# Kernel tuning notes

Hardware: AMD Instinct MI355X
Metric: run time of the kernel (lower is better)

Reference implementation:

```python
import jax, jax.numpy as jnp
import numpy as np

HID = 128  # hidden_channel
C = 256    # feat_channel

def conv1x1(x, w, b):
    # x: [N, Cin, H, W], w: [Cout, Cin], b: [Cout]
    return jnp.einsum('nchw,oc->nohw', x, w) + b[None, :, None, None]

def maxpool2(x):
    N, Ch, H, W = x.shape
    return x.reshape(N, Ch, H // 2, 2, W // 2, 2).max(axis=(3, 5))

def setup_inputs() -> dict:
    key = jax.random.key(0)
    ks = jax.random.split(key, 6)
    rois = jax.random.normal(ks[0], (128, C, 14, 14), dtype=jnp.float32)
    feature = jax.random.normal(ks[1], (2, C, 64, 64), dtype=jnp.float32)
    s_in = 1.0 / np.sqrt(C)
    s_hid = 1.0 / np.sqrt(HID)
    wq = jax.random.uniform(ks[2], (HID, C), minval=-s_in, maxval=s_in, dtype=jnp.float32)
    wk = jax.random.uniform(ks[3], (HID, C), minval=-s_in, maxval=s_in, dtype=jnp.float32)
    wv = jax.random.uniform(ks[4], (HID, C), minval=-s_in, maxval=s_in, dtype=jnp.float32)
    wre = jax.random.uniform(ks[5], (C, HID), minval=-s_hid, maxval=s_hid, dtype=jnp.float32)
    return {
        'rois': rois, 'feature': feature,
        'wq': wq, 'bq': jnp.zeros((HID,), jnp.float32),
        'wk': wk, 'bk': jnp.zeros((HID,), jnp.float32),
        'wv': wv, 'bv': jnp.zeros((HID,), jnp.float32),
        'wre': wre, 'bre': jnp.zeros((C,), jnp.float32),
    }

def reference(rois, feature, wq, bq, wk, bk, wv, bv, wre, bre):
    BS_roinum, Cf, h, w = rois.shape
    BS = feature.shape[0]
    roinum = BS_roinum // BS
    _h, _w = h // 2, w // 2

    # Q at full resolution
    q = conv1x1(rois, wq, bq)                              # [BS*R, HID, h, w]
    q = q.transpose(0, 2, 3, 1).reshape(BS, roinum * h * w, HID)

    ds = maxpool2(rois)                                    # [BS*R, C, _h, _w]
    k = conv1x1(ds, wk, bk).transpose(0, 2, 3, 1).reshape(BS, roinum * _h * _w, HID)
    v = conv1x1(ds, wv, bv).transpose(0, 2, 3, 1).reshape(BS, roinum * _h * _w, HID)

    score = jnp.einsum('bqc,bkc->bqk', q, k)               # [BS, R*h*w, R*_h*_w]
    score = jax.nn.softmax(score, axis=-1)
    y = jnp.einsum('bqk,bkc->bqc', score, v)               # [BS, R*h*w, HID]

    y = y.reshape(BS * roinum, h, w, HID).transpose(0, 3, 1, 2)
    y = conv1x1(y, wre, bre)                               # [BS*R, C, h, w]
    return rois + y
```

## Files before the change

### kernel.cpp

```cpp
#include <hip/hip_runtime.h>
#include <math.h>

constexpr int CIN  = 256;
constexpr int HID  = 128;
constexpr int P    = 196;
constexpr int PP   = 49;
constexpr int NQ   = 12544;
constexpr int NKEY = 3136;
constexpr int NS   = 5;

using f32x4 = __attribute__((ext_vector_type(4))) float;
using s16x8 = __attribute__((ext_vector_type(8))) short;
using s16x4 = __attribute__((ext_vector_type(4))) short;
using u32x2 = __attribute__((ext_vector_type(2))) unsigned int;

#define GLOBAL_AS(p) ((const void __attribute__((address_space(1)))*)(p))
#define LDS_AS(p)    ((void __attribute__((address_space(3)))*)(p))

__device__ __forceinline__ unsigned short f2bf(float x) {
    unsigned int u = __float_as_uint(x);
    u += 0x7FFFu + ((u >> 16) & 1u);
    return (unsigned short)(u >> 16);
}
__device__ __forceinline__ float bf2f(unsigned short s) {
    return __uint_as_float(((unsigned int)s) << 16);
}

__global__ __launch_bounds__(256) void prep_kernel(
    const float* __restrict__ rois,
    const float* __restrict__ wq, const float* __restrict__ wk,
    const float* __restrict__ wv, const float* __restrict__ wre,
    unsigned short* __restrict__ xkv,
    unsigned short* __restrict__ wqb, unsigned short* __restrict__ wkb,
    unsigned short* __restrict__ wvb, unsigned short* __restrict__ wreb)
{
    const int bx = blockIdx.x;
    const int t  = threadIdx.x;

    if (bx >= 512) {
        const int which = bx - 512;
        const float* src = (which == 0) ? wq : (which == 1) ? wk : (which == 2) ? wv : wre;
        unsigned short* dst = (which == 0) ? wqb : (which == 1) ? wkb
                             : (which == 2) ? wvb : wreb;
        #pragma unroll 4
        for (int i = 0; i < 32; ++i) {
            const int idx = i * 256 + t;
            const float4 v = ((const float4*)src)[idx];
            s16x4 o;
            o[0] = (short)f2bf(v.x); o[1] = (short)f2bf(v.y);
            o[2] = (short)f2bf(v.z); o[3] = (short)f2bf(v.w);
            *(s16x4*)(dst + idx * 4) = o;
        }
        return;
    }

    const int n = bx >> 2;
    const int g = bx & 3;
    const int b = n >> 6, r = n & 63;
    __shared__ float xT[196 * 68];

    const int c_loc = t >> 2;
    const int pq    = t & 3;

    const float4* row4 = (const float4*)(rois + ((size_t)n * CIN + g * 64 + c_loc) * P);
    #pragma unroll
    for (int j = 0; j < 13; ++j) {
        const int idx4 = pq + 4 * j;
        if (idx4 < 49) {
            const float4 v = row4[idx4];
            xT[(idx4 * 4 + 0) * 68 + c_loc] = v.x;
            xT[(idx4 * 4 + 1) * 68 + c_loc] = v.y;
            xT[(idx4 * 4 + 2) * 68 + c_loc] = v.z;
            xT[(idx4 * 4 + 3) * 68 + c_loc] = v.w;
        }
    }
    __syncthreads();

    #pragma unroll
    for (int i = 0; i < 2; ++i) {
        const int u = i * 256 + t;
        if (u < 392) {
            const int pp = u >> 3, ch8 = (u & 7) * 8;
            const int py = pp / 7, px_ = pp - py * 7;
            const int base00 = (py * 2) * 14 + px_ * 2;
            s16x8 o;
            #pragma unroll
            for (int e = 0; e < 8; ++e) {
                const int c = ch8 + e;
                const float m0 = fmaxf(xT[(base00)      * 68 + c], xT[(base00 + 1)  * 68 + c]);
                const float m1 = fmaxf(xT[(base00 + 14) * 68 + c], xT[(base00 + 15) * 68 + c]);
                o[e] = (short)f2bf(fmaxf(m0, m1));
            }
            *(s16x8*)(xkv + ((size_t)b * NKEY + r * PP + pp) * CIN + g * 64 + ch8) = o;
        }
    }
}

__global__ __launch_bounds__(128) void gemm_fused_kernel(
    const float* __restrict__ rois, const unsigned short* __restrict__ xkv,
    const unsigned short* __restrict__ wqb, const unsigned short* __restrict__ wkb,
    const unsigned short* __restrict__ wvb,
    const float* __restrict__ bq, const float* __restrict__ bk, const float* __restrict__ bv,
    unsigned short* __restrict__ q, unsigned short* __restrict__ kmat,
    unsigned short* __restrict__ vt_g)
{
    const int bx = blockIdx.x;
    const int t = threadIdx.x;
    const int wid = t >> 6, lane = t & 63;
    const int quad = lane >> 4, c = lane & 15;

    __shared__ unsigned short xT[64 * 264];

    f32x4 acc[4][4];
    #pragma unroll
    for (int i = 0; i < 4; ++i)
        #pragma unroll
        for (int j = 0; j < 4; ++j) acc[i][j] = (f32x4)(0.f);

    if (bx < 392) {
        const int m0 = bx * 64;
        {
            const int c_loc = t >> 2;
            const int pq4   = t & 3;
            const int sw    = pq4 << 3;
            #pragma unroll
            for (int ci = 0; ci < 8; ++ci) {
                const int ch = ci * 32 + c_loc;
                #pragma unroll
                for (int j = 0; j < 4; ++j) {
                    const int idx4 = (m0 >> 2) + pq4 + 4 * j;
                    const int n_img = idx4 / 49;
                    const int p4 = idx4 - n_img * 49;
                    const float4 v = ((const float4*)(rois + ((size_t)(n_img * CIN + ch)) * P))[p4];
                    const int r0 = (pq4 + 4 * j) * 4;
                    const int cs = ch ^ sw;
                    xT[(r0 + 0) * 264 + cs] = f2bf(v.x);
                    xT[(r0 + 1) * 264 + cs] = f2bf(v.y);
                    xT[(r0 + 2) * 264 + cs] = f2bf(v.z);
                    xT[(r0 + 3) * 264 + cs] = f2bf(v.w);
                }
            }
        }
        __syncthreads();

        const int m_base = m0;
        const int n_base = wid * 64;
        const int swr = ((c >> 2) & 3) << 3;
        #pragma unroll
        for (int ks = 0; ks < 8; ++ks) {
            s16x8 af[4], bf[4];
            #pragma unroll
            for (int mt = 0; mt < 4; ++mt)
                af[mt] = *(const s16x8*)&xT[(mt * 16 + c) * 264 + ((ks * 32 + quad * 8) ^ swr)];
            #pragma unroll
            for (int nt = 0; nt < 4; ++nt)
                bf[nt] = *(const s16x8*)(wqb + (size_t)(n_base + nt * 16 + c) * CIN + ks * 32 + quad * 8);
            #pragma unroll
            for (int mt = 0; mt < 4; ++mt)
                #pragma unroll
                for (int nt = 0; nt < 4; ++nt)
                    acc[mt][nt] = __builtin_amdgcn_mfma_f32_16x16x32_bf16(bf[nt], af[mt], acc[mt][nt], 0, 0, 0);
        }
        #pragma unroll
        for (int mt = 0; mt < 4; ++mt) {
            const int m = m_base + mt * 16 + c;
            #pragma unroll
            for (int nt = 0; nt < 4; ++nt) {
                const int n0 = n_base + nt * 16 + quad * 4;
                const float4 b4 = *(const float4*)&bq[n0];
                s16x4 o4;
                o4[0] = (short)f2bf(acc[mt][nt][0] + b4.x);
                o4[1] = (short)f2bf(acc[mt][nt][1] + b4.y);
                o4[2] = (short)f2bf(acc[mt][nt][2] + b4.z);
                o4[3] = (short)f2bf(acc[mt][nt][3] + b4.w);
                *(s16x4*)(q + (size_t)m * HID + n0) = o4;
            }
        }
        return;
    }

    const unsigned short* w; const float* bias;
    int m_blk, mode;
    if (bx < 490) { mode = 1; w = wkb; bias = bk; m_blk = bx - 392; }
    else          { mode = 2; w = wvb; bias = bv; m_blk = bx - 490; }
    const int m_base = m_blk * 64;
    const int n_base = wid * 64;

    if (mode == 1) {
        #pragma unroll
        for (int ks = 0; ks < 8; ++ks) {
            s16x8 af[4], bf[4];
            #pragma unroll
            for (int mt = 0; mt < 4; ++mt)
                af[mt] = *(const s16x8*)(xkv + (size_t)(m_base + mt * 16 + c) * CIN + ks * 32 + quad * 8);
            #pragma unroll
            for (int nt = 0; nt < 4; ++nt)
                bf[nt] = *(const s16x8*)(w + (size_t)(n_base + nt * 16 + c) * CIN + ks * 32 + quad * 8);
            #pragma unroll
            for (int mt = 0; mt < 4; ++mt)
                #pragma unroll
                for (int nt = 0; nt < 4; ++nt)
                    acc[mt][nt] = __builtin_amdgcn_mfma_f32_16x16x32_bf16(bf[nt], af[mt], acc[mt][nt], 0, 0, 0);
        }
        #pragma unroll
        for (int mt = 0; mt < 4; ++mt) {
            const int m = m_base + mt * 16 + c;
            #pragma unroll
            for (int nt = 0; nt < 4; ++nt) {
                const int n0 = n_base + nt * 16 + quad * 4;
                const float4 b4 = *(const float4*)&bias[n0];
                s16x4 o4;
                o4[0] = (short)f2bf(acc[mt][nt][0] + b4.x);
                o4[1] = (short)f2bf(acc[mt][nt][1] + b4.y);
                o4[2] = (short)f2bf(acc[mt][nt][2] + b4.z);
                o4[3] = (short)f2bf(acc[mt][nt][3] + b4.w);
                *(s16x4*)(kmat + (size_t)m * HID + n0) = o4;
            }
        }
    } else {
        #pragma unroll
        for (int ks = 0; ks < 8; ++ks) {
            s16x8 af[4], bf[4];
            #pragma unroll
            for (int mt = 0; mt < 4; ++mt)
                af[mt] = *(const s16x8*)(xkv + (size_t)(m_base + mt * 16 + c) * CIN + ks * 32 + quad * 8);
            #pragma unroll
            for (int nt = 0; nt < 4; ++nt)
                bf[nt] = *(const s16x8*)(w + (size_t)(n_base + nt * 16 + c) * CIN + ks * 32 + quad * 8);
            #pragma unroll
            for (int mt = 0; mt < 4; ++mt)
                #pragma unroll
                for (int nt = 0; nt < 4; ++nt)
                    acc[mt][nt] = __builtin_amdgcn_mfma_f32_16x16x32_bf16(af[mt], bf[nt], acc[mt][nt], 0, 0, 0);
        }
        #pragma unroll
        for (int nt = 0; nt < 4; ++nt) {
            const int d = n_base + nt * 16 + c;
            const float bv_ = bias[d];
            #pragma unroll
            for (int mt = 0; mt < 4; ++mt) {
                const int key0 = m_base + mt * 16 + quad * 4;
                const int bb = (key0 >= NKEY) ? 1 : 0;
                const int kl = key0 - bb * NKEY;
                s16x4 o4;
                #pragma unroll
                for (int rr = 0; rr < 4; ++rr)
                    o4[rr] = (short)f2bf(acc[mt][nt][rr] + bv_);
                *(s16x4*)(vt_g + ((size_t)bb * HID + d) * NKEY + kl) = o4;
            }
        }
    }
}

__global__ __launch_bounds__(256, 2) void attn_kernel(
    const unsigned short* __restrict__ q, const unsigned short* __restrict__ kmat,
    const unsigned short* __restrict__ vt_g,
    unsigned short* __restrict__ opart, float* __restrict__ lpart)
{
    const int fid  = blockIdx.x;
    const int xcd  = fid & 7, slot = fid >> 3;
    const int wg   = (xcd < 2 ? xcd * 62 : 124 + (xcd - 2) * 61) + slot;
    const int g    = wg / NS;
    const int s    = wg - g * NS;
    const int qblk = g % 49;
    const int b    = g / 49;

    const int tid  = threadIdx.x;
    const int w    = tid >> 6;
    const int lane = tid & 63;
    const int quad = lane >> 4;
    const int c    = lane & 15;
    const int qb   = qblk * 256 + w * 64;

    __shared__ unsigned short Kst[2][32 * 128];
    __shared__ unsigned short Vst[2][128 * 32];
    __shared__ unsigned short Ps[4][64 * 72];

    const unsigned short* qg = q    + (size_t)b * NQ   * HID;
    const unsigned short* kg = kmat + (size_t)b * NKEY * HID;
    const unsigned short* vt = vt_g + (size_t)b * HID  * NKEY;

    int koff[2], voff[2];
    #pragma unroll
    for (int i = 0; i < 2; ++i) {
        const int dstk = w * 2048 + (i * 64 + lane) * 16;
        koff[i] = dstk ^ (((dstk >> 8) & 7) << 4);
        const int chunk = i * 64 + lane;
        const int d = w * 32 + (chunk >> 2), sl = chunk & 3;
        voff[i] = d * (NKEY * 2) + ((sl ^ (d & 3)) * 16);
    }
    const char* kc = (const char*)kg;
    const char* vc = (const char*)vt;

    const int B6[6] = {0, 20, 40, 60, 79, 98};
    const int kt0 = B6[s], kt1 = B6[s + 1];

    {
        const char* ks_ = kc + (size_t)kt0 * 8192;
        const char* vs_ = vc + (size_t)kt0 * 64;
        #pragma unroll
        for (int i = 0; i < 2; ++i) {
            __builtin_amdgcn_global_load_lds(GLOBAL_AS(ks_ + koff[i]),
                LDS_AS((char*)&Kst[0][0] + w * 2048 + i * 1024), 16, 0, 0);
            __builtin_amdgcn_global_load_lds(GLOBAL_AS(vs_ + voff[i]),
                LDS_AS((char*)&Vst[0][0] + w * 2048 + i * 1024), 16, 0, 0);
        }
    }

    s16x8 qf[4][4];
    #pragma unroll
    for (int nt = 0; nt < 4; ++nt)
        #pragma unroll
        for (int ks = 0; ks < 4; ++ks)
            qf[nt][ks] = *(const s16x8*)(qg + (size_t)(qb + nt * 16 + c) * HID + ks * 32 + quad * 8);

    f32x4 Ob[4][8];
    #pragma unroll
    for (int nt = 0; nt < 4; ++nt)
        #pragma unroll
        for (int nd = 0; nd < 8; ++nd) Ob[nt][nd] = (f32x4)(0.f);
    float l[4] = {0.f, 0.f, 0.f, 0.f};

    __syncthreads();

    int buf = 0;
    for (int kt = kt0; kt < kt1; ++kt) {
        if (kt + 1 < kt1) {
            const char* ks_ = kc + (size_t)(kt + 1) * 8192;
            const char* vs_ = vc + (size_t)(kt + 1) * 64;
            #pragma unroll
            for (int i = 0; i < 2; ++i) {
                __builtin_amdgcn_global_load_lds(GLOBAL_AS(ks_ + koff[i]),
                    LDS_AS((char*)&Kst[buf ^ 1][0] + w * 2048 + i * 1024), 16, 0, 0);
                __builtin_amdgcn_global_load_lds(GLOBAL_AS(vs_ + voff[i]),
                    LDS_AS((char*)&Vst[buf ^ 1][0] + w * 2048 + i * 1024), 16, 0, 0);
            }
        }

        const char* Kb = (const char*)&Kst[buf][0];
        const char* Vb = (const char*)&Vst[buf][0];

        f32x4 st[2][4];
        #pragma unroll
        for (int mt = 0; mt < 2; ++mt)
            #pragma unroll
            for (int nt = 0; nt < 4; ++nt) st[mt][nt] = (f32x4)(0.f);
        #pragma unroll
        for (int mt = 0; mt < 2; ++mt) {
            const int row = mt * 16 + c;
            s16x8 kf[4];
            #pragma unroll
            for (int ks = 0; ks < 4; ++ks)
                kf[ks] = *(const s16x8*)(Kb + ((row * 256 + ks * 64 + quad * 16) ^ ((c & 7) << 4)));
            #pragma unroll
            for (int ks = 0; ks < 4; ++ks)
                #pragma unroll
                for (int nt = 0; nt < 4; ++nt)
                    st[mt][nt] = __builtin_amdgcn_mfma_f32_16x16x32_bf16(kf[ks], qf[nt][ks], st[mt][nt], 0, 0, 0);
        }

        #pragma unroll
        for (int mt = 0; mt < 2; ++mt) {
            #pragma unroll
            for (int nt = 0; nt < 4; ++nt) {
                const float e0 = __expf(st[mt][nt][0]);
                const float e1 = __expf(st[mt][nt][1]);
                const float e2 = __expf(st[mt][nt][2]);
                const float e3 = __expf(st[mt][nt][3]);
                l[nt] += (e0 + e1) + (e2 + e3);
                u32x2 pk;
                pk[0] = (unsigned int)f2bf(e0) | ((unsigned int)f2bf(e1) << 16);
                pk[1] = (unsigned int)f2bf(e2) | ((unsigned int)f2bf(e3) << 16);
                *(u32x2*)&Ps[w][(nt * 16 + c) * 72 + mt * 16 + quad * 4] = pk;
            }
        }

        s16x8 pf[4];
        #pragma unroll
        for (int nt = 0; nt < 4; ++nt)
            pf[nt] = *(const s16x8*)&Ps[w][(nt * 16 + c) * 72 + quad * 8];
        #pragma unroll
        for (int g2 = 0; g2 < 2; ++g2) {
            s16x8 vf[4];
            #pragma unroll
            for (int dd = 0; dd < 4; ++dd) {
                const int d = (g2 * 4 + dd) * 16 + c;
                vf[dd] = *(const s16x8*)(Vb + (d * 64 + ((quad ^ (d & 3)) * 16)));
            }
            #pragma unroll
            for (int dd = 0; dd < 4; ++dd)
                #pragma unroll
                for (int nt = 0; nt < 4; ++nt)
                    Ob[nt][g2 * 4 + dd] = __builtin_amdgcn_mfma_f32_16x16x32_bf16(pf[nt], vf[dd], Ob[nt][g2 * 4 + dd], 0, 0, 0);
        }

        if (kt + 1 < kt1) __syncthreads();
        buf ^= 1;
    }

    unsigned short* Op = opart + (size_t)(s * 2 + b) * NQ * HID;
    #pragma unroll
    for (int nt = 0; nt < 4; ++nt) {
        #pragma unroll
        for (int nd = 0; nd < 8; ++nd) {
            #pragma unroll
            for (int rr = 0; rr < 4; ++rr) {
                const int qrow = qb + nt * 16 + quad * 4 + rr;
                Op[(size_t)qrow * HID + nd * 16 + c] = f2bf(Ob[nt][nd][rr]);
            }
        }
    }
    #pragma unroll
    for (int nt = 0; nt < 4; ++nt) {
        l[nt] += __shfl_xor(l[nt], 16, 64);
        l[nt] += __shfl_xor(l[nt], 32, 64);
    }
    if (quad == 0) {
        float* lp = lpart + (size_t)(s * 2 + b) * NQ;
        #pragma unroll
        for (int nt = 0; nt < 4; ++nt) lp[qb + nt * 16 + c] = l[nt];
    }
}

__global__ __launch_bounds__(256) void outproj_kernel(
    const float* __restrict__ rois,
    const unsigned short* __restrict__ opart, const float* __restrict__ lpart,
    const unsigned short* __restrict__ wreb, const float* __restrict__ bre,
    float* __restrict__ out)
{
    const int t = threadIdx.x;
    const int wid = t >> 6, lane = t & 63;
    const int quad = lane >> 4, c = lane & 15;
    const int m0 = blockIdx.x * 64;
    const int b  = (m0 >= NQ) ? 1 : 0;

    __shared__ unsigned short ys[64 * 136];

    {
        const int m_loc = t >> 2, kq = t & 3;
        const int q_local = (m0 + m_loc) - b * NQ;
        float lsum = 0.f;
        #pragma unroll
        for (int sl = 0; sl < NS; ++sl)
            lsum += lpart[(size_t)(sl * 2 + b) * NQ + q_local];
        const float invl = 1.0f / lsum;
        #pragma unroll
        for (int ch = 0; ch < 4; ++ch) {
            float a8[8] = {0, 0, 0, 0, 0, 0, 0, 0};
            #pragma unroll
            for (int sl = 0; sl < NS; ++sl) {
                const s16x8 v = *(const s16x8*)&opart[
                    ((size_t)(sl * 2 + b) * NQ + q_local) * HID + kq * 32 + ch * 8];
                #pragma unroll
                for (int e = 0; e < 8; ++e) a8[e] += bf2f((unsigned short)v[e]);
            }
            s16x8 o;
            #pragma unroll
            for (int e = 0; e < 8; ++e) o[e] = (short)f2bf(a8[e] * invl);
            *(s16x8*)&ys[m_loc * 136 + kq * 32 + ch * 8] = o;
        }
    }
    __syncthreads();

    const int o_base = wid * 64;
    s16x8 wf[4][4];
    #pragma unroll
    for (int ot = 0; ot < 4; ++ot)
        #pragma unroll
        for (int ks = 0; ks < 4; ++ks)
            wf[ot][ks] = *(const s16x8*)(wreb + (size_t)(o_base + ot * 16 + c) * HID + ks * 32 + quad * 8);

    f32x4 acc[4][4];
    #pragma unroll
    for (int i = 0; i < 4; ++i)
        #pragma unroll
        for (int j = 0; j < 4; ++j) acc[i][j] = (f32x4)(0.f);

    #pragma unroll
    for (int ks = 0; ks < 4; ++ks) {
        s16x8 yf[4];
        #pragma unroll
        for (int mt = 0; mt < 4; ++mt)
            yf[mt] = *(const s16x8*)&ys[(mt * 16 + c) * 136 + ks * 32 + quad * 8];
        #pragma unroll
        for (int mt = 0; mt < 4; ++mt)
            #pragma unroll
            for (int ot = 0; ot < 4; ++ot)
                acc[mt][ot] = __builtin_amdgcn_mfma_f32_16x16x32_bf16(yf[mt], wf[ot][ks], acc[mt][ot], 0, 0, 0);
    }

    #pragma unroll
    for (int ot = 0; ot < 4; ++ot) {
        const int o = o_base + ot * 16 + c;
        const float br = bre[o];
        #pragma unroll
        for (int mt = 0; mt < 4; ++mt) {
            const int m_g = m0 + mt * 16 + quad * 4;
            const int mm  = m_g - b * NQ;
            const int r_roi = mm / 196;
            const int p     = mm - r_roi * 196;
            const int n_img = b * 64 + r_roi;
            const size_t base = ((size_t)n_img * CIN + o) * P + p;
            const float4 rv = *(const float4*)&rois[base];
            float4 ov;
            ov.x = rv.x + br + acc[mt][ot][0];
            ov.y = rv.y + br + acc[mt][ot][1];
            ov.z = rv.z + br + acc[mt][ot][2];
            ov.w = rv.w + br + acc[mt][ot][3];
            *(float4*)&out[base] = ov;
        }
    }
}

extern "C" void kernel_launch(void* const* d_in, const int* in_sizes, int n_in,
                              void* d_out, int out_size, void* d_ws, size_t ws_size,
                              hipStream_t stream)
{
    (void)in_sizes; (void)n_in; (void)out_size; (void)ws_size;
    const float* rois = (const float*)d_in[0];
    const float* wq  = (const float*)d_in[2];
    const float* bq  = (const float*)d_in[3];
    const float* wk  = (const float*)d_in[4];
    const float* bk  = (const float*)d_in[5];
    const float* wv  = (const float*)d_in[6];
    const float* bv  = (const float*)d_in[7];
    const float* wre = (const float*)d_in[8];
    const float* bre = (const float*)d_in[9];
    float* out = (float*)d_out;

    char* ws = (char*)d_ws;
    unsigned short* opart = (unsigned short*)(ws);
    unsigned short* xkv   = (unsigned short*)(ws + 12845056);
    unsigned short* wqb   = (unsigned short*)(ws + 16056320);
    unsigned short* wkb   = (unsigned short*)(ws + 16121856);
    unsigned short* wvb   = (unsigned short*)(ws + 16187392);
    unsigned short* q     = (unsigned short*)(ws + 32112640);
    unsigned short* kmat  = (unsigned short*)(ws + 38535168);
    unsigned short* vt_g  = (unsigned short*)(ws + 40140800);
    float*          lpart = (float*)         (ws + 41746432);
    unsigned short* wreb  = (unsigned short*)(ws + 42248192);

    prep_kernel<<<dim3(516), 256, 0, stream>>>(rois, wq, wk, wv, wre,
                                               xkv, wqb, wkb, wvb, wreb);
    gemm_fused_kernel<<<dim3(588), 128, 0, stream>>>(rois, xkv, wqb, wkb, wvb,
                                                     bq, bk, bv, q, kmat, vt_g);
    attn_kernel<<<dim3(490), 256, 0, stream>>>(q, kmat, vt_g, opart, lpart);
    outproj_kernel<<<dim3(392), 256, 0, stream>>>(rois, opart, lpart, wreb, bre, out);
}
```

Baseline: 191.2 us.

## Fuse maxpool and weight conversion into projection GEMM kernel, drop prep launch

Removes the separate prep kernel. The K/V projection blocks now max-pool one ROI directly from fp32 rois into swizzled LDS, and every GEMM converts fp32 weights to bf16 on the fly, while one extra block converts wre. This saves a kernel launch and the global round trip through the pooled xkv buffer. In exchange, weight bf16 conversion is repeated in every block, K/V tiles of 49 rows waste part of the 64-row MFMA tile, and the V-transpose stores become scalar.

```diff
diff --git a/kernel.cpp b/kernel.cpp
--- a/kernel.cpp
+++ b/kernel.cpp
@@ -26,86 +26,30 @@
     return __uint_as_float(((unsigned int)s) << 16);
 }
 
-__global__ __launch_bounds__(256) void prep_kernel(
+__global__ __launch_bounds__(128) void gemm_fused_kernel(
     const float* __restrict__ rois,
     const float* __restrict__ wq, const float* __restrict__ wk,
     const float* __restrict__ wv, const float* __restrict__ wre,
-    unsigned short* __restrict__ xkv,
-    unsigned short* __restrict__ wqb, unsigned short* __restrict__ wkb,
-    unsigned short* __restrict__ wvb, unsigned short* __restrict__ wreb)
+    const float* __restrict__ bq, const float* __restrict__ bk, const float* __restrict__ bv,
+    unsigned short* __restrict__ q, unsigned short* __restrict__ kmat,
+    unsigned short* __restrict__ vt_g, unsigned short* __restrict__ wreb)
 {
     const int bx = blockIdx.x;
-    const int t  = threadIdx.x;
-
-    if (bx >= 512) {
-        const int which = bx - 512;
-        const float* src = (which == 0) ? wq : (which == 1) ? wk : (which == 2) ? wv : wre;
-        unsigned short* dst = (which == 0) ? wqb : (which == 1) ? wkb
-                             : (which == 2) ? wvb : wreb;
+    const int t = threadIdx.x;
+
+    if (bx == 648) {
         #pragma unroll 4
-        for (int i = 0; i < 32; ++i) {
-            const int idx = i * 256 + t;
-            const float4 v = ((const float4*)src)[idx];
+        for (int i = 0; i < 64; ++i) {
+            const int idx = i * 128 + t;
+            const float4 v = ((const float4*)wre)[idx];
             s16x4 o;
             o[0] = (short)f2bf(v.x); o[1] = (short)f2bf(v.y);
             o[2] = (short)f2bf(v.z); o[3] = (short)f2bf(v.w);
-            *(s16x4*)(dst + idx * 4) = o;
+            *(s16x4*)(wreb + idx * 4) = o;
         }
         return;
     }
 
-    const int n = bx >> 2;
-    const int g = bx & 3;
-    const int b = n >> 6, r = n & 63;
-    __shared__ float xT[196 * 68];
-
-    const int c_loc = t >> 2;
-    const int pq    = t & 3;
-
-    const float4* row4 = (const float4*)(rois + ((size_t)n * CIN + g * 64 + c_loc) * P);
-    #pragma unroll
-    for (int j = 0; j < 13; ++j) {
-        const int idx4 = pq + 4 * j;
-        if (idx4 < 49) {
-            const float4 v = row4[idx4];
-            xT[(idx4 * 4 + 0) * 68 + c_loc] = v.x;
-            xT[(idx4 * 4 + 1) * 68 + c_loc] = v.y;
-            xT[(idx4 * 4 + 2) * 68 + c_loc] = v.z;
-            xT[(idx4 * 4 + 3) * 68 + c_loc] = v.w;
-        }
-    }
-    __syncthreads();
-
-    #pragma unroll
-    for (int i = 0; i < 2; ++i) {
-        const int u = i * 256 + t;
-        if (u < 392) {
-            const int pp = u >> 3, ch8 = (u & 7) * 8;
-            const int py = pp / 7, px_ = pp - py * 7;
-            const int base00 = (py * 2) * 14 + px_ * 2;
-            s16x8 o;
-            #pragma unroll
-            for (int e = 0; e < 8; ++e) {
-                const int c = ch8 + e;
-                const float m0 = fmaxf(xT[(base00)      * 68 + c], xT[(base00 + 1)  * 68 + c]);
-                const float m1 = fmaxf(xT[(base00 + 14) * 68 + c], xT[(base00 + 15) * 68 + c]);
-                o[e] = (short)f2bf(fmaxf(m0, m1));
-            }
-            *(s16x8*)(xkv + ((size_t)b * NKEY + r * PP + pp) * CIN + g * 64 + ch8) = o;
-        }
-    }
-}
-
-__global__ __launch_bounds__(128) void gemm_fused_kernel(
-    const float* __restrict__ rois, const unsigned short* __restrict__ xkv,
-    const unsigned short* __restrict__ wqb, const unsigned short* __restrict__ wkb,
-    const unsigned short* __restrict__ wvb,
-    const float* __restrict__ bq, const float* __restrict__ bk, const float* __restrict__ bv,
-    unsigned short* __restrict__ q, unsigned short* __restrict__ kmat,
-    unsigned short* __restrict__ vt_g)
-{
-    const int bx = blockIdx.x;
-    const int t = threadIdx.x;
     const int wid = t >> 6, lane = t & 63;
     const int quad = lane >> 4, c = lane & 15;
 
@@ -116,6 +60,9 @@
     for (int i = 0; i < 4; ++i)
         #pragma unroll
         for (int j = 0; j < 4; ++j) acc[i][j] = (f32x4)(0.f);
+
+    const int n_base = wid * 64;
+    const int swr = ((c >> 2) & 3) << 3;
 
     if (bx < 392) {
         const int m0 = bx * 64;
@@ -143,9 +90,6 @@
         }
         __syncthreads();
 
-        const int m_base = m0;
-        const int n_base = wid * 64;
-        const int swr = ((c >> 2) & 3) << 3;
         #pragma unroll
         for (int ks = 0; ks < 8; ++ks) {
             s16x8 af[4], bf[4];
@@ -153,8 +97,17 @@
             for (int mt = 0; mt < 4; ++mt)
                 af[mt] = *(const s16x8*)&xT[(mt * 16 + c) * 264 + ((ks * 32 + quad * 8) ^ swr)];
             #pragma unroll
-            for (int nt = 0; nt < 4; ++nt)
-                bf[nt] = *(const s16x8*)(wqb + (size_t)(n_base + nt * 16 + c) * CIN + ks * 32 + quad * 8);
+            for (int nt = 0; nt < 4; ++nt) {
+                const float* wp = wq + (size_t)(n_base + nt * 16 + c) * CIN + ks * 32 + quad * 8;
+                const float4 w0 = *(const float4*)wp;
+                const float4 w1 = *(const float4*)(wp + 4);
+                s16x8 bv8;
+                bv8[0] = (short)f2bf(w0.x); bv8[1] = (short)f2bf(w0.y);
+                bv8[2] = (short)f2bf(w0.z); bv8[3] = (short)f2bf(w0.w);
+                bv8[4] = (short)f2bf(w1.x); bv8[5] = (short)f2bf(w1.y);
+                bv8[6] = (short)f2bf(w1.z); bv8[7] = (short)f2bf(w1.w);
+                bf[nt] = bv8;
+            }
             #pragma unroll
             for (int mt = 0; mt < 4; ++mt)
                 #pragma unroll
@@ -163,7 +116,7 @@
         }
         #pragma unroll
         for (int mt = 0; mt < 4; ++mt) {
-            const int m = m_base + mt * 16 + c;
+            const int m = m0 + mt * 16 + c;
             #pragma unroll
             for (int nt = 0; nt < 4; ++nt) {
                 const int n0 = n_base + nt * 16 + quad * 4;
@@ -179,12 +132,28 @@
         return;
     }
 
-    const unsigned short* w; const float* bias;
-    int m_blk, mode;
-    if (bx < 490) { mode = 1; w = wkb; bias = bk; m_blk = bx - 392; }
-    else          { mode = 2; w = wvb; bias = bv; m_blk = bx - 490; }
-    const int m_base = m_blk * 64;
-    const int n_base = wid * 64;
+    const int mode = (bx < 520) ? 1 : 2;
+    const int n_roi = bx - ((mode == 1) ? 392 : 520);
+    const int b = n_roi >> 6, r = n_roi & 63;
+    {
+        #pragma unroll
+        for (int i = 0; i < 16; ++i) {
+            const int unit = i * 128 + t;
+            const int ch = unit >> 3, py = unit & 7;
+            if (py < 7) {
+                const float* ra = rois + ((size_t)n_roi * CIN + ch) * P + py * 28;
+                #pragma unroll
+                for (int px = 0; px < 7; ++px) {
+                    const float2 a = *(const float2*)(ra + px * 2);
+                    const float2 bb = *(const float2*)(ra + 14 + px * 2);
+                    const float m = fmaxf(fmaxf(a.x, a.y), fmaxf(bb.x, bb.y));
+                    const int pp = py * 7 + px;
+                    xT[pp * 264 + (ch ^ (((pp >> 2) & 3) << 3))] = f2bf(m);
+                }
+            }
+        }
+    }
+    __syncthreads();
 
     if (mode == 1) {
         #pragma unroll
@@ -192,10 +161,19 @@
             s16x8 af[4], bf[4];
             #pragma unroll
             for (int mt = 0; mt < 4; ++mt)
-                af[mt] = *(const s16x8*)(xkv + (size_t)(m_base + mt * 16 + c) * CIN + ks * 32 + quad * 8);
-            #pragma unroll
-            for (int nt = 0; nt < 4; ++nt)
-                bf[nt] = *(const s16x8*)(w + (size_t)(n_base + nt * 16 + c) * CIN + ks * 32 + quad * 8);
+                af[mt] = *(const s16x8*)&xT[(mt * 16 + c) * 264 + ((ks * 32 + quad * 8) ^ swr)];
+            #pragma unroll
+            for (int nt = 0; nt < 4; ++nt) {
+                const float* wp = wk + (size_t)(n_base + nt * 16 + c) * CIN + ks * 32 + quad * 8;
+                const float4 w0 = *(const float4*)wp;
+                const float4 w1 = *(const float4*)(wp + 4);
+                s16x8 bv8;
+                bv8[0] = (short)f2bf(w0.x); bv8[1] = (short)f2bf(w0.y);
+                bv8[2] = (short)f2bf(w0.z); bv8[3] = (short)f2bf(w0.w);
+                bv8[4] = (short)f2bf(w1.x); bv8[5] = (short)f2bf(w1.y);
+                bv8[6] = (short)f2bf(w1.z); bv8[7] = (short)f2bf(w1.w);
+                bf[nt] = bv8;
+            }
             #pragma unroll
             for (int mt = 0; mt < 4; ++mt)
                 #pragma unroll
@@ -204,17 +182,20 @@
         }
         #pragma unroll
         for (int mt = 0; mt < 4; ++mt) {
-            const int m = m_base + mt * 16 + c;
-            #pragma unroll
-            for (int nt = 0; nt < 4; ++nt) {
-                const int n0 = n_base + nt * 16 + quad * 4;
-                const float4 b4 = *(const float4*)&bias[n0];
-                s16x4 o4;
-                o4[0] = (short)f2bf(acc[mt][nt][0] + b4.x);
-                o4[1] = (short)f2bf(acc[mt][nt][1] + b4.y);
-                o4[2] = (short)f2bf(acc[mt][nt][2] + b4.z);
-                o4[3] = (short)f2bf(acc[mt][nt][3] + b4.w);
-                *(s16x4*)(kmat + (size_t)m * HID + n0) = o4;
+            const int m = mt * 16 + c;
+            if (mt < 3 || c == 0) {
+                const size_t krow = (size_t)(b * NKEY + r * 49 + m) * HID;
+                #pragma unroll
+                for (int nt = 0; nt < 4; ++nt) {
+                    const int n0 = n_base + nt * 16 + quad * 4;
+                    const float4 b4 = *(const float4*)&bk[n0];
+                    s16x4 o4;
+                    o4[0] = (short)f2bf(acc[mt][nt][0] + b4.x);
+                    o4[1] = (short)f2bf(acc[mt][nt][1] + b4.y);
+                    o4[2] = (short)f2bf(acc[mt][nt][2] + b4.z);
+                    o4[3] = (short)f2bf(acc[mt][nt][3] + b4.w);
+                    *(s16x4*)(kmat + krow + n0) = o4;
+                }
             }
         }
     } else {
@@ -223,10 +204,19 @@
             s16x8 af[4], bf[4];
             #pragma unroll
             for (int mt = 0; mt < 4; ++mt)
-                af[mt] = *(const s16x8*)(xkv + (size_t)(m_base + mt * 16 + c) * CIN + ks * 32 + quad * 8);
-            #pragma unroll
-            for (int nt = 0; nt < 4; ++nt)
-                bf[nt] = *(const s16x8*)(w + (size_t)(n_base + nt * 16 + c) * CIN + ks * 32 + quad * 8);
+                af[mt] = *(const s16x8*)&xT[(mt * 16 + c) * 264 + ((ks * 32 + quad * 8) ^ swr)];
+            #pragma unroll
+            for (int nt = 0; nt < 4; ++nt) {
+                const float* wp = wv + (size_t)(n_base + nt * 16 + c) * CIN + ks * 32 + quad * 8;
+                const float4 w0 = *(const float4*)wp;
+                const float4 w1 = *(const float4*)(wp + 4);
+                s16x8 bv8;
+                bv8[0] = (short)f2bf(w0.x); bv8[1] = (short)f2bf(w0.y);
+                bv8[2] = (short)f2bf(w0.z); bv8[3] = (short)f2bf(w0.w);
+                bv8[4] = (short)f2bf(w1.x); bv8[5] = (short)f2bf(w1.y);
+                bv8[6] = (short)f2bf(w1.z); bv8[7] = (short)f2bf(w1.w);
+                bf[nt] = bv8;
+            }
             #pragma unroll
             for (int mt = 0; mt < 4; ++mt)
                 #pragma unroll
@@ -236,17 +226,18 @@
         #pragma unroll
         for (int nt = 0; nt < 4; ++nt) {
             const int d = n_base + nt * 16 + c;
-            const float bv_ = bias[d];
+            const float bv_ = bv[d];
+            const size_t vrow = ((size_t)b * HID + d) * NKEY + r * 49;
             #pragma unroll
             for (int mt = 0; mt < 4; ++mt) {
-                const int key0 = m_base + mt * 16 + quad * 4;
-                const int bb = (key0 >= NKEY) ? 1 : 0;
-                const int kl = key0 - bb * NKEY;
-                s16x4 o4;
-                #pragma unroll
-                for (int rr = 0; rr < 4; ++rr)
-                    o4[rr] = (short)f2bf(acc[mt][nt][rr] + bv_);
-                *(s16x4*)(vt_g + ((size_t)bb * HID + d) * NKEY + kl) = o4;
+                const int key0 = mt * 16 + quad * 4;
+                if (mt < 3) {
+                    #pragma unroll
+                    for (int rr = 0; rr < 4; ++rr)
+                        vt_g[vrow + key0 + rr] = f2bf(acc[mt][nt][rr] + bv_);
+                } else if (quad == 0) {
+                    vt_g[vrow + 48] = f2bf(acc[mt][nt][0] + bv_);
+                }
             }
         }
     }
@@ -530,20 +521,14 @@
 
     char* ws = (char*)d_ws;
     unsigned short* opart = (unsigned short*)(ws);
-    unsigned short* xkv   = (unsigned short*)(ws + 12845056);
-    unsigned short* wqb   = (unsigned short*)(ws + 16056320);
-    unsigned short* wkb   = (unsigned short*)(ws + 16121856);
-    unsigned short* wvb   = (unsigned short*)(ws + 16187392);
     unsigned short* q     = (unsigned short*)(ws + 32112640);
     unsigned short* kmat  = (unsigned short*)(ws + 38535168);
     unsigned short* vt_g  = (unsigned short*)(ws + 40140800);
     float*          lpart = (float*)         (ws + 41746432);
     unsigned short* wreb  = (unsigned short*)(ws + 42248192);
 
-    prep_kernel<<<dim3(516), 256, 0, stream>>>(rois, wq, wk, wv, wre,
-                                               xkv, wqb, wkb, wvb, wreb);
-    gemm_fused_kernel<<<dim3(588), 128, 0, stream>>>(rois, xkv, wqb, wkb, wvb,
-                                                     bq, bk, bv, q, kmat, vt_g);
+    gemm_fused_kernel<<<dim3(649), 128, 0, stream>>>(rois, wq, wk, wv, wre,
+                                                     bq, bk, bv, q, kmat, vt_g, wreb);
     attn_kernel<<<dim3(490), 256, 0, stream>>>(q, kmat, vt_g, opart, lpart);
     outproj_kernel<<<dim3(392), 256, 0, stream>>>(rois, opart, lpart, wreb, bre, out);
 }
```

New measurement: 194.6 us. Within noise of the previous version (+1.8%).
